# Kernel tuning notes

Hardware: AMD Instinct MI355X
Metric: run time of the kernel (lower is better)

Reference implementation:

```python
import jax, jax.numpy as jnp
import numpy as np

N, E, IN, H, C, OUT = 100000, 800000, 256, 4, 32, 64
NEG_SLOPE = 0.2


def _glorot(key, shape):
    fan = shape[0] if len(shape) > 1 else shape[-1]
    return jax.random.normal(key, shape, dtype=jnp.float32) * (1.0 / np.sqrt(fan))


def setup_inputs() -> dict:
    key = jax.random.key(0)
    ks = jax.random.split(key, 24)
    inp = {
        'x': jax.random.normal(ks[0], (N, IN), dtype=jnp.float32),
        'edge_index': jax.random.randint(ks[1], (2, E), 0, N, dtype=jnp.int64),
        # GATConv layer 0: 256 -> 4 heads x 32 (concat -> 128)
        'W0': _glorot(ks[2], (IN, H * C)), 'b0': jnp.zeros((H * C,), jnp.float32),
        'as0': _glorot(ks[3], (H, C)), 'ad0': _glorot(ks[4], (H, C)),
        # GATConv layer 1: 128 -> 4 heads x 32 (concat -> 128)
        'W1': _glorot(ks[5], (H * C, H * C)), 'b1': jnp.zeros((H * C,), jnp.float32),
        'as1': _glorot(ks[6], (H, C)), 'ad1': _glorot(ks[7], (H, C)),
        # GATConv layer 2: 128 -> 1 head x 64 (mean, concat=False)
        'W2': _glorot(ks[8], (H * C, OUT)), 'b2': jnp.zeros((OUT,), jnp.float32),
        'as2': _glorot(ks[9], (1, OUT)), 'ad2': _glorot(ks[10], (1, OUT)),
        # skip projections: layer0 Linear(256->128), layer1 Identity, layer2 Linear(128->64)
        'skip0_W': _glorot(ks[11], (IN, H * C)), 'skip0_b': jnp.zeros((H * C,), jnp.float32),
        'skip2_W': _glorot(ks[12], (H * C, OUT)), 'skip2_b': jnp.zeros((OUT,), jnp.float32),
        # JK concat linear: (128+128+64) -> 64
        'jk_W': _glorot(ks[13], (2 * H * C + OUT, OUT)), 'jk_b': jnp.zeros((OUT,), jnp.float32),
    }
    return inp


def gat_layer(x, src, dst, n, W, b, a_src, a_dst, heads, concat):
    # x: [N, F_in]; src/dst: [E'] (self-loops included); W: [F_in, heads*C]
    xh = (x @ W).reshape(n, heads, -1)                    # [N, H, C]
    al_src = jnp.einsum('nhc,hc->nh', xh, a_src)          # [N, H]
    al_dst = jnp.einsum('nhc,hc->nh', xh, a_dst)
    e = jax.nn.leaky_relu(al_src[src] + al_dst[dst], NEG_SLOPE)   # [E', H]
    emax = jax.ops.segment_max(e, dst, num_segments=n)    # self-loops => every segment nonempty
    w = jnp.exp(e - emax[dst])                            # [E', H]
    denom = jax.ops.segment_sum(w, dst, num_segments=n)   # [N, H]
    msg = xh[src] * w[:, :, None]                         # [E', H, C]
    out = jax.ops.segment_sum(msg, dst, num_segments=n) / denom[:, :, None]
    if concat:
        return out.reshape(n, -1) + b
    return out.mean(axis=1) + b


def reference(x, edge_index, W0, b0, as0, ad0, W1, b1, as1, ad1, W2, b2, as2, ad2,
              skip0_W, skip0_b, skip2_W, skip2_b, jk_W, jk_b):
    n = x.shape[0]
    loops = jnp.arange(n, dtype=edge_index.dtype)
    src = jnp.concatenate([edge_index[0], loops])
    dst = jnp.concatenate([edge_index[1], loops])
    # layer 0 (dropout is identity in eval mode)
    res0 = x @ skip0_W + skip0_b
    h = gat_layer(x, src, dst, n, W0, b0, as0, ad0, H, True) + res0
    h = jax.nn.elu(h)
    x0 = h
    # layer 1 (skip proj is Identity: 128 == 128)
    h = gat_layer(h, src, dst, n, W1, b1, as1, ad1, H, True) + h
    h = jax.nn.elu(h)
    x1 = h
    # layer 2 (1 head, concat=False -> head mean; no ELU)
    res2 = h @ skip2_W + skip2_b
    h = gat_layer(h, src, dst, n, W2, b2, as2, ad2, 1, False) + res2
    # JumpingKnowledge 'cat' + linear
    jk = jnp.concatenate([x0, x1, h], axis=-1)            # [N, 320]
    return jk @ jk_W + jk_b                               # [N, 64]
```

## Files before the change

### kernel.cpp

```cpp
#include <hip/hip_runtime.h>
#include <hip/hip_bf16.h>
#include <cstdint>

static constexpr int NN = 100000;
static constexpr int NE = 800000;
static constexpr int EP = NE + NN;
static constexpr int NB = (NN + 255) / 256;

typedef unsigned short ushort;
typedef __attribute__((ext_vector_type(8))) short short8;
typedef __attribute__((ext_vector_type(8))) ushort ushort8v;
typedef __attribute__((ext_vector_type(4))) float f32x4;

__device__ __forceinline__ float leaky(float x) { return x > 0.f ? x : 0.2f * x; }

__device__ __forceinline__ ushort f2bf(float f) {
    unsigned int u = __float_as_uint(f);
    u += 0x7fffu + ((u >> 16) & 1u);
    return (ushort)(u >> 16);
}
__device__ __forceinline__ float bf2f(ushort h) {
    return __uint_as_float(((unsigned int)h) << 16);
}

__device__ __forceinline__ void gload16(const void* g, void* l) {
    __builtin_amdgcn_global_load_lds((__attribute__((address_space(1))) void*)g,
                                     (__attribute__((address_space(3))) void*)l,
                                     16, 0, 0);
}

__global__ void pretile_kernel(const float* __restrict__ Wa, const float* __restrict__ Wb,
                               int K, int CS, int NT,
                               ushort* __restrict__ Whi, ushort* __restrict__ Wlo)
{
    int idx = blockIdx.x * 256 + threadIdx.x;
    if (idx >= K * NT) return;
    int k = idx / NT, c = idx - k * NT;
    float v = (c < CS) ? Wa[(size_t)k * CS + c] : Wb[(size_t)k * (NT - CS) + (c - CS)];
    ushort h = f2bf(v);
    ushort l = f2bf(v - bf2f(h));
    size_t o = ((size_t)(k >> 5) * NT + c) * 32 + (k & 31);
    Whi[o] = h; Wlo[o] = l;
}

template<int KTOT, int NTOT, int K1, int K2, int CSPLIT, int BIAS_OFF,
         int AHH, int ACC, int ATTN, bool ASPLIT, int MINW>
__global__ __launch_bounds__(256, MINW)
void gemm_mfma(const void* __restrict__ X1, const void* __restrict__ X1b,
               const void* __restrict__ X2, const void* __restrict__ X2b,
               const void* __restrict__ X3, const void* __restrict__ X3b,
               int ldx1, int ldx2, int ldx3,
               const ushort* __restrict__ Wthi, const ushort* __restrict__ Wtlo,
               const float* __restrict__ bias,
               float* __restrict__ Y1, float* __restrict__ Y2, int ldy1, int ldy2,
               float* __restrict__ als, float* __restrict__ ald,
               const float* __restrict__ a_src, const float* __restrict__ a_dst,
               int n)
{
    constexpr int NKT = KTOT / 32;
    constexpr int NF  = NTOT / 16;

    __shared__ ushort Bh[2][NTOT * 32], Bl[2][NTOT * 32];

    const int t = threadIdx.x, l = t & 63, w = t >> 6;
    const int lc = l & 15, lq = l >> 4;
    const int wrow = blockIdx.x * 128 + w * 32;

    f32x4 acc[2][NF];
#pragma unroll
    for (int mf = 0; mf < 2; ++mf)
#pragma unroll
        for (int nf = 0; nf < NF; ++nf)
            acc[mf][nf] = (f32x4){0.f, 0.f, 0.f, 0.f};

    int  arow[2]; bool aval[2];
#pragma unroll
    for (int mf = 0; mf < 2; ++mf) {
        arow[mf] = wrow + mf * 16 + lc;
        aval[mf] = arow[mf] < n;
    }

    short8 A0h[2], A0l[2], A1h[2], A1l[2];
    float4 F0[2][2], F1[2][2];

    auto loadA = [&](int kt, short8 (&dh)[2], short8 (&dl)[2], float4 (&df)[2][2]) {
        const int k0 = kt * 32;
        const void* xp; const void* xq; int ldx, koff;
        if (k0 < K1)      { xp = X1; xq = X1b; ldx = ldx1; koff = k0; }
        else if (k0 < K2) { xp = X2; xq = X2b; ldx = ldx2; koff = k0 - K1; }
        else              { xp = X3; xq = X3b; ldx = ldx3; koff = k0 - K2; }
        if constexpr (ASPLIT) {
            const ushort* ph = (const ushort*)xp;
            const ushort* pl = (const ushort*)xq;
#pragma unroll
            for (int mf = 0; mf < 2; ++mf) {
                short8 zh = {0,0,0,0,0,0,0,0}, zl = {0,0,0,0,0,0,0,0};
                if (aval[mf]) {
                    size_t o = (size_t)arow[mf] * ldx + koff + lq * 8;
                    zh = *(const short8*)&ph[o];
                    zl = *(const short8*)&pl[o];
                }
                dh[mf] = zh; dl[mf] = zl;
            }
        } else {
            const float* pf = (const float*)xp;
#pragma unroll
            for (int mf = 0; mf < 2; ++mf) {
                float4 za = make_float4(0.f,0.f,0.f,0.f), zb = za;
                if (aval[mf]) {
                    size_t o = (size_t)arow[mf] * ldx + koff + lq * 8;
                    za = *(const float4*)&pf[o];
                    zb = *(const float4*)&pf[o + 4];
                }
                df[mf][0] = za; df[mf][1] = zb;
            }
        }
    };

    auto stageB = [&](int kt, int buf) {
        constexpr int UN = NTOT * 4;
#pragma unroll
        for (int s = 0; s < UN / 256; ++s) {
            int unit = s * 256 + t;
            int col  = unit & (NTOT - 1);
            int kq   = unit / NTOT;
            size_t go = ((size_t)kt * NTOT + col) * 32 + kq * 8;
            gload16(&Wthi[go], &Bh[buf][unit * 8]);
            gload16(&Wtlo[go], &Bl[buf][unit * 8]);
        }
    };

    loadA(0, A0h, A0l, F0);
    stageB(0, 0);
    __syncthreads();

#pragma unroll
    for (int kt = 0; kt < NKT; ++kt) {
        if (kt + 1 < NKT) {
            if (((kt + 1) & 1) == 0) loadA(kt + 1, A0h, A0l, F0);
            else                     loadA(kt + 1, A1h, A1l, F1);
            stageB(kt + 1, (kt + 1) & 1);
        }

        short8 ah[2], al[2];
        if constexpr (ASPLIT) {
            if ((kt & 1) == 0) { ah[0]=A0h[0]; ah[1]=A0h[1]; al[0]=A0l[0]; al[1]=A0l[1]; }
            else               { ah[0]=A1h[0]; ah[1]=A1h[1]; al[0]=A1l[0]; al[1]=A1l[1]; }
        } else {
            const auto& Fc = (kt & 1) ? F1 : F0;
#pragma unroll
            for (int mf = 0; mf < 2; ++mf) {
                short8 h8, l8;
#pragma unroll
                for (int e = 0; e < 8; ++e) {
                    float f = (e < 4) ? (&Fc[mf][0].x)[e] : (&Fc[mf][1].x)[e - 4];
                    ushort hh = f2bf(f);
                    h8[e] = (short)hh;
                    l8[e] = (short)f2bf(f - bf2f(hh));
                }
                ah[mf] = h8; al[mf] = l8;
            }
        }

        const int cb = kt & 1;
#pragma unroll
        for (int nf = 0; nf < NF; ++nf) {
            int bslot = lq * NTOT + nf * 16 + lc;
            short8 bh = *(const short8*)&Bh[cb][bslot * 8];
            short8 bl = *(const short8*)&Bl[cb][bslot * 8];
#pragma unroll
            for (int mf = 0; mf < 2; ++mf) {
                acc[mf][nf] = __builtin_amdgcn_mfma_f32_16x16x32_bf16(ah[mf], bh, acc[mf][nf], 0, 0, 0);
                acc[mf][nf] = __builtin_amdgcn_mfma_f32_16x16x32_bf16(ah[mf], bl, acc[mf][nf], 0, 0, 0);
                acc[mf][nf] = __builtin_amdgcn_mfma_f32_16x16x32_bf16(al[mf], bh, acc[mf][nf], 0, 0, 0);
            }
        }
        __syncthreads();
    }

    if constexpr (AHH > 0) {
        constexpr int FPH = ACC / 16;
        constexpr int NG  = ATTN / ACC;
#pragma unroll
        for (int g = 0; g < NG; ++g) {
#pragma unroll
            for (int mf = 0; mf < 2; ++mf) {
                float ps[4] = {0.f, 0.f, 0.f, 0.f};
                float pd[4] = {0.f, 0.f, 0.f, 0.f};
#pragma unroll
                for (int j = 0; j < FPH; ++j) {
                    int col = g * ACC + j * 16 + lc;
                    float av = a_src[col], dv = a_dst[col];
#pragma unroll
                    for (int r = 0; r < 4; ++r) {
                        ps[r] = fmaf(acc[mf][g * FPH + j][r], av, ps[r]);
                        pd[r] = fmaf(acc[mf][g * FPH + j][r], dv, pd[r]);
                    }
                }
#pragma unroll
                for (int off = 1; off < 16; off <<= 1)
#pragma unroll
                    for (int r = 0; r < 4; ++r) {
                        ps[r] += __shfl_xor(ps[r], off);
                        pd[r] += __shfl_xor(pd[r], off);
                    }
                if (lc == 0) {
#pragma unroll
                    for (int r = 0; r < 4; ++r) {
                        int row = wrow + mf * 16 + lq * 4 + r;
                        if (row < n) {
                            als[(size_t)row * AHH + g] = ps[r];
                            ald[(size_t)row * AHH + g] = pd[r];
                        }
                    }
                }
            }
        }
    }

#pragma unroll
    for (int mf = 0; mf < 2; ++mf) {
        int rb4 = wrow + mf * 16 + lq * 4;
#pragma unroll
        for (int nf = 0; nf < NF; ++nf) {
            int col = nf * 16 + lc;
            float bv = 0.f;
            if constexpr (BIAS_OFF < NTOT) {
                if (col >= BIAS_OFF) bv = bias[col - BIAS_OFF];
            }
#pragma unroll
            for (int r = 0; r < 4; ++r) {
                int row = rb4 + r;
                if (row < n) {
                    float v = acc[mf][nf][r] + bv;
                    if (col < CSPLIT)
                        Y1[(size_t)row * ldy1 + col] = v;
                    else
                        Y2[(size_t)row * ldy2 + (col - CSPLIT)] = v;
                }
            }
        }
    }
}

__global__ void deg_kernel(const int* __restrict__ ei, int* __restrict__ deg)
{
    int t = blockIdx.x * blockDim.x + threadIdx.x;
    if (t < NE) atomicAdd(&deg[ei[NE + t]], 1);
}

__global__ void block_sum_kernel(const int* __restrict__ deg, int* __restrict__ bsum)
{
    int node = blockIdx.x * 256 + threadIdx.x;
    int v = (node < NN) ? deg[node] + 1 : 0;
#pragma unroll
    for (int off = 32; off > 0; off >>= 1) v += __shfl_down(v, off);
    __shared__ int sh[4];
    if ((threadIdx.x & 63) == 0) sh[threadIdx.x >> 6] = v;
    __syncthreads();
    if (threadIdx.x == 0) bsum[blockIdx.x] = sh[0] + sh[1] + sh[2] + sh[3];
}

__global__ void scan_sums_kernel(const int* __restrict__ bsum, int* __restrict__ bsumx,
                                 int* __restrict__ rowptr)
{
    if (threadIdx.x == 0) {
        int run = 0;
        for (int i = 0; i < NB; ++i) { bsumx[i] = run; run += bsum[i]; }
        rowptr[NN] = run;
    }
}

__global__ void scan_blocks_kernel(const int* __restrict__ deg, const int* __restrict__ bsumx,
                                   int* __restrict__ rowptr, int* __restrict__ cursor)
{
    __shared__ int sh[256];
    int node = blockIdx.x * 256 + threadIdx.x;
    int v = (node < NN) ? deg[node] + 1 : 0;
    sh[threadIdx.x] = v;
    __syncthreads();
#pragma unroll
    for (int off = 1; off < 256; off <<= 1) {
        int tv = (threadIdx.x >= off) ? sh[threadIdx.x - off] : 0;
        __syncthreads();
        sh[threadIdx.x] += tv;
        __syncthreads();
    }
    if (node < NN) {
        int excl = bsumx[blockIdx.x] + sh[threadIdx.x] - v;
        rowptr[node] = excl;
        cursor[node] = excl;
    }
}

__global__ void fill_kernel(const int* __restrict__ ei, int* __restrict__ cursor,
                            int* __restrict__ csr_src)
{
    int t = blockIdx.x * blockDim.x + threadIdx.x;
    if (t >= EP) return;
    int s, d;
    if (t < NE) { s = ei[t]; d = ei[NE + t]; }
    else        { s = d = t - NE; }
    int pos = atomicAdd(&cursor[d], 1);
    csr_src[pos] = s;
}

template<int HH>
__global__ __launch_bounds__(256)
void attn_weights_kernel(const int* __restrict__ rowptr, const int* __restrict__ csr_src,
                         const float* __restrict__ als, const float* __restrict__ ald,
                         float* __restrict__ wq, int n)
{
    int node = blockIdx.x * 256 + threadIdx.x;
    if (node >= n) return;
    const int e0 = rowptr[node], e1 = rowptr[node + 1];
    float aldv[HH], m[HH], d[HH];
#pragma unroll
    for (int h = 0; h < HH; ++h) { m[h] = -1e30f; d[h] = 0.f; }
    if constexpr (HH == 4) {
        float4 a = *(const float4*)&ald[(size_t)node * 4];
        aldv[0] = a.x; aldv[1] = a.y; aldv[2] = a.z; aldv[3] = a.w;
    } else {
        aldv[0] = ald[node];
    }
    for (int e = e0; e < e1; ++e) {
        int s = csr_src[e];
        float av[HH];
        if constexpr (HH == 4) {
            float4 a = *(const float4*)&als[(size_t)s * 4];
            av[0] = a.x; av[1] = a.y; av[2] = a.z; av[3] = a.w;
        } else {
            av[0] = als[s];
        }
#pragma unroll
        for (int h = 0; h < HH; ++h) {
            float sc = leaky(av[h] + aldv[h]);
            float nm = fmaxf(m[h], sc);
            d[h] = d[h] * __expf(m[h] - nm) + __expf(sc - nm);
            m[h] = nm;
        }
    }
#pragma unroll
    for (int h = 0; h < HH; ++h) d[h] = 1.f / d[h];
    for (int e = e0; e < e1; ++e) {
        int s = csr_src[e];
        float av[HH];
        if constexpr (HH == 4) {
            float4 a = *(const float4*)&als[(size_t)s * 4];
            av[0] = a.x; av[1] = a.y; av[2] = a.z; av[3] = a.w;
        } else {
            av[0] = als[s];
        }
        float wv[HH];
#pragma unroll
        for (int h = 0; h < HH; ++h)
            wv[h] = __expf(leaky(av[h] + aldv[h]) - m[h]) * d[h];
        if constexpr (HH == 4) {
            float4 o; o.x = wv[0]; o.y = wv[1]; o.z = wv[2]; o.w = wv[3];
            *(float4*)&wq[(size_t)e * 4] = o;
        } else {
            wq[e] = wv[0];
        }
    }
}

template<int HH, int CC, bool DOELU, bool RESSPLIT>
__global__ __launch_bounds__(256)
void spmm_kernel(const int* __restrict__ rowptr, const int* __restrict__ csr_src,
                 const float* __restrict__ xh, const float* __restrict__ wq,
                 const float* __restrict__ b,
                 const float* __restrict__ resf,
                 const ushort* __restrict__ resh, const ushort* __restrict__ resl,
                 ushort* __restrict__ outh, ushort* __restrict__ outl, int n)
{
    constexpr int HCL = HH * CC;
    constexpr int CPL = HCL / 64;
    const int l = threadIdx.x & 63;
    const int node = blockIdx.x * 4 + (threadIdx.x >> 6);
    if (node >= n) return;
    const int c = l * CPL;
    const int h = c / CC;
    const int e0 = rowptr[node], e1 = rowptr[node + 1];

    float a0[CPL], a1[CPL];
#pragma unroll
    for (int j = 0; j < CPL; ++j) { a0[j] = 0.f; a1[j] = 0.f; }

    int e = e0;
    for (; e + 1 < e1; e += 2) {
        int s0 = csr_src[e], s1 = csr_src[e + 1];
        float w0 = wq[(size_t)e * HH + h];
        float w1 = wq[(size_t)(e + 1) * HH + h];
        if constexpr (CPL == 2) {
            float2 x0 = *(const float2*)&xh[(size_t)s0 * HCL + c];
            float2 x1 = *(const float2*)&xh[(size_t)s1 * HCL + c];
            a0[0] = fmaf(w0, x0.x, a0[0]); a0[1] = fmaf(w0, x0.y, a0[1]);
            a1[0] = fmaf(w1, x1.x, a1[0]); a1[1] = fmaf(w1, x1.y, a1[1]);
        } else {
            a0[0] = fmaf(w0, xh[(size_t)s0 * HCL + c], a0[0]);
            a1[0] = fmaf(w1, xh[(size_t)s1 * HCL + c], a1[0]);
        }
    }
    if (e < e1) {
        int s0 = csr_src[e];
        float w0 = wq[(size_t)e * HH + h];
        if constexpr (CPL == 2) {
            float2 x0 = *(const float2*)&xh[(size_t)s0 * HCL + c];
            a0[0] = fmaf(w0, x0.x, a0[0]); a0[1] = fmaf(w0, x0.y, a0[1]);
        } else {
            a0[0] = fmaf(w0, xh[(size_t)s0 * HCL + c], a0[0]);
        }
    }

#pragma unroll
    for (int j = 0; j < CPL; ++j) {
        size_t idx = (size_t)node * HCL + c + j;
        float rv;
        if constexpr (RESSPLIT) rv = bf2f(resh[idx]) + bf2f(resl[idx]);
        else                    rv = resf[idx];
        float v = a0[j] + a1[j] + b[c + j] + rv;
        if (DOELU) v = v > 0.f ? v : (__expf(v) - 1.f);
        ushort hh = f2bf(v);
        outh[idx] = hh;
        outl[idx] = f2bf(v - bf2f(hh));
    }
}

extern "C" void kernel_launch(void* const* d_in, const int* in_sizes, int n_in,
                              void* d_out, int out_size, void* d_ws, size_t ws_size,
                              hipStream_t stream)
{
    const float* x    = (const float*)d_in[0];
    const int*   ei   = (const int*)d_in[1];
    const float* W0   = (const float*)d_in[2];
    const float* b0   = (const float*)d_in[3];
    const float* as0  = (const float*)d_in[4];
    const float* ad0  = (const float*)d_in[5];
    const float* W1   = (const float*)d_in[6];
    const float* b1   = (const float*)d_in[7];
    const float* as1  = (const float*)d_in[8];
    const float* ad1  = (const float*)d_in[9];
    const float* W2   = (const float*)d_in[10];
    const float* b2   = (const float*)d_in[11];
    const float* as2  = (const float*)d_in[12];
    const float* ad2  = (const float*)d_in[13];
    const float* sk0W = (const float*)d_in[14];
    const float* sk0b = (const float*)d_in[15];
    const float* sk2W = (const float*)d_in[16];
    const float* sk2b = (const float*)d_in[17];
    const float* jkW  = (const float*)d_in[18];
    const float* jkb  = (const float*)d_in[19];
    float* out = (float*)d_out;

    float* ws = (float*)d_ws;
    size_t off = 0;
    float* s_xh  = ws + off; off += (size_t)NN * 128;
    float* s_r0  = ws + off; off += (size_t)NN * 128;
    float* s_als = ws + off; off += (size_t)NN * 4;
    float* s_ald = ws + off; off += (size_t)NN * 4;
    float* f_wq  = ws + off; off += (size_t)EP * 4;
    ushort* u_x0h = (ushort*)(ws + off); off += (size_t)NN * 64;
    ushort* u_x0l = (ushort*)(ws + off); off += (size_t)NN * 64;
    ushort* u_x1h = (ushort*)(ws + off); off += (size_t)NN * 64;
    ushort* u_x1l = (ushort*)(ws + off); off += (size_t)NN * 64;
    ushort* u_h2h = (ushort*)(ws + off); off += (size_t)NN * 32;
    ushort* u_h2l = (ushort*)(ws + off); off += (size_t)NN * 32;
    int* i_deg    = (int*)(ws + off); off += NN;
    int* i_rowptr = (int*)(ws + off); off += NN + 1;
    int* i_cursor = (int*)(ws + off); off += NN;
    int* i_csrsrc = (int*)(ws + off); off += EP;
    int* i_bsum   = (int*)(ws + off); off += NB;
    int* i_bsumx  = (int*)(ws + off); off += NB;
    off = (off + 3) & ~(size_t)3;
    ushort* wt0h = (ushort*)(ws + off); off += 32768;
    ushort* wt0l = (ushort*)(ws + off); off += 32768;
    ushort* wt1h = (ushort*)(ws + off); off += 8192;
    ushort* wt1l = (ushort*)(ws + off); off += 8192;
    ushort* wt2h = (ushort*)(ws + off); off += 8192;
    ushort* wt2l = (ushort*)(ws + off); off += 8192;
    ushort* wtjh = (ushort*)(ws + off); off += 10240;
    ushort* wtjl = (ushort*)(ws + off); off += 10240;

    const int G128 = (NN + 127) / 128;
    const int GN = (NN + 255) / 256;
    const int GS = (NN + 3) / 4;
    constexpr int BIG = 1 << 30;

    hipMemsetAsync(i_deg, 0, (size_t)NN * sizeof(int), stream);
    deg_kernel<<<(NE + 255) / 256, 256, 0, stream>>>(ei, i_deg);
    block_sum_kernel<<<NB, 256, 0, stream>>>(i_deg, i_bsum);
    scan_sums_kernel<<<1, 64, 0, stream>>>(i_bsum, i_bsumx, i_rowptr);
    scan_blocks_kernel<<<NB, 256, 0, stream>>>(i_deg, i_bsumx, i_rowptr, i_cursor);
    fill_kernel<<<(EP + 255) / 256, 256, 0, stream>>>(ei, i_cursor, i_csrsrc);

    pretile_kernel<<<256, 256, 0, stream>>>(W0, sk0W, 256, 128, 256, wt0h, wt0l);
    pretile_kernel<<<64,  256, 0, stream>>>(W1, nullptr, 128, 128, 128, wt1h, wt1l);
    pretile_kernel<<<64,  256, 0, stream>>>(W2, sk2W, 128, 64, 128, wt2h, wt2l);
    pretile_kernel<<<80,  256, 0, stream>>>(jkW, nullptr, 320, 64, 64, wtjh, wtjl);

    gemm_mfma<256, 256, 256, 256, 128, 128, 4, 32, 128, false, 2>
        <<<G128, 256, 0, stream>>>(
        x, nullptr, nullptr, nullptr, nullptr, nullptr, 256, 0, 0,
        wt0h, wt0l, sk0b,
        s_xh, s_r0, 128, 128, s_als, s_ald, as0, ad0, NN);
    attn_weights_kernel<4><<<GN, 256, 0, stream>>>(
        i_rowptr, i_csrsrc, s_als, s_ald, f_wq, NN);
    spmm_kernel<4, 32, true, false><<<GS, 256, 0, stream>>>(
        i_rowptr, i_csrsrc, s_xh, f_wq, b0, s_r0, nullptr, nullptr,
        u_x0h, u_x0l, NN);

    gemm_mfma<128, 128, 128, 128, 128, BIG, 4, 32, 128, true, 3>
        <<<G128, 256, 0, stream>>>(
        u_x0h, u_x0l, nullptr, nullptr, nullptr, nullptr, 128, 0, 0,
        wt1h, wt1l, nullptr,
        s_xh, nullptr, 128, 0, s_als, s_ald, as1, ad1, NN);
    attn_weights_kernel<4><<<GN, 256, 0, stream>>>(
        i_rowptr, i_csrsrc, s_als, s_ald, f_wq, NN);
    spmm_kernel<4, 32, true, true><<<GS, 256, 0, stream>>>(
        i_rowptr, i_csrsrc, s_xh, f_wq, b1, nullptr, u_x0h, u_x0l,
        u_x1h, u_x1l, NN);

    gemm_mfma<128, 128, 128, 128, 64, 64, 1, 64, 64, true, 3>
        <<<G128, 256, 0, stream>>>(
        u_x1h, u_x1l, nullptr, nullptr, nullptr, nullptr, 128, 0, 0,
        wt2h, wt2l, sk2b,
        s_xh, s_r0, 64, 64, s_als, s_ald, as2, ad2, NN);
    attn_weights_kernel<1><<<GN, 256, 0, stream>>>(
        i_rowptr, i_csrsrc, s_als, s_ald, f_wq, NN);
    spmm_kernel<1, 64, false, false><<<GS, 256, 0, stream>>>(
        i_rowptr, i_csrsrc, s_xh, f_wq, b2, s_r0, nullptr, nullptr,
        u_h2h, u_h2l, NN);

    gemm_mfma<320, 64, 128, 256, 64, 0, 0, 16, 0, true, 3>
        <<<G128, 256, 0, stream>>>(
        u_x0h, u_x0l, u_x1h, u_x1l, u_h2h, u_h2l, 128, 128, 64,
        wtjh, wtjl, jkb,
        out, nullptr, 64, 0, nullptr, nullptr, nullptr, nullptr, NN);
}
```

Measured before the change: 647.4 us.

## Use partial vmcnt wait barriers so A-prefetch stays in flight across k-tiles

Reorders each k-step so the B tile global->LDS loads are issued before the A register prefetch. The full __syncthreads is replaced by an s_waitcnt vmcnt(4) plus s_barrier, which waits only for the B loads and lets the four A loads for the next tile stay outstanding while the MFMAs run. Out-of-range rows are clamped to n-1 instead of branching, so the load count is uniform and the vmcnt arithmetic holds. The risk is that the hardcoded count of 4 must match the number of A loads per tile. Clamped rows also read real data that must be discarded at store time.

After: 628.6 us. 1.03x faster.

```diff
diff --git a/kernel.cpp b/kernel.cpp
--- a/kernel.cpp
+++ b/kernel.cpp
@@ -27,6 +27,12 @@
     __builtin_amdgcn_global_load_lds((__attribute__((address_space(1))) void*)g,
                                      (__attribute__((address_space(3))) void*)l,
                                      16, 0, 0);
+}
+
+__device__ __forceinline__ void waitbar4() {
+    asm volatile("s_waitcnt vmcnt(4)" ::: "memory");
+    __builtin_amdgcn_s_barrier();
+    __builtin_amdgcn_sched_barrier(0);
 }
 
 __global__ void pretile_kernel(const float* __restrict__ Wa, const float* __restrict__ Wb,
@@ -73,11 +79,11 @@
         for (int nf = 0; nf < NF; ++nf)
             acc[mf][nf] = (f32x4){0.f, 0.f, 0.f, 0.f};
 
-    int  arow[2]; bool aval[2];
+    int arow[2], rcl[2];
 #pragma unroll
     for (int mf = 0; mf < 2; ++mf) {
         arow[mf] = wrow + mf * 16 + lc;
-        aval[mf] = arow[mf] < n;
+        rcl[mf]  = arow[mf] < n ? arow[mf] : (n - 1);
     }
 
     short8 A0h[2], A0l[2], A1h[2], A1l[2];
@@ -94,25 +100,17 @@
             const ushort* pl = (const ushort*)xq;
 #pragma unroll
             for (int mf = 0; mf < 2; ++mf) {
-                short8 zh = {0,0,0,0,0,0,0,0}, zl = {0,0,0,0,0,0,0,0};
-                if (aval[mf]) {
-                    size_t o = (size_t)arow[mf] * ldx + koff + lq * 8;
-                    zh = *(const short8*)&ph[o];
-                    zl = *(const short8*)&pl[o];
-                }
-                dh[mf] = zh; dl[mf] = zl;
+                size_t o = (size_t)rcl[mf] * ldx + koff + lq * 8;
+                dh[mf] = *(const short8*)&ph[o];
+                dl[mf] = *(const short8*)&pl[o];
             }
         } else {
             const float* pf = (const float*)xp;
 #pragma unroll
             for (int mf = 0; mf < 2; ++mf) {
-                float4 za = make_float4(0.f,0.f,0.f,0.f), zb = za;
-                if (aval[mf]) {
-                    size_t o = (size_t)arow[mf] * ldx + koff + lq * 8;
-                    za = *(const float4*)&pf[o];
-                    zb = *(const float4*)&pf[o + 4];
-                }
-                df[mf][0] = za; df[mf][1] = zb;
+                size_t o = (size_t)rcl[mf] * ldx + koff + lq * 8;
+                df[mf][0] = *(const float4*)&pf[o];
+                df[mf][1] = *(const float4*)&pf[o + 4];
             }
         }
     };
@@ -130,16 +128,18 @@
         }
     };
 
+    stageB(0, 0);
+    __builtin_amdgcn_sched_barrier(0);
     loadA(0, A0h, A0l, F0);
-    stageB(0, 0);
-    __syncthreads();
+    waitbar4();
 
 #pragma unroll
     for (int kt = 0; kt < NKT; ++kt) {
         if (kt + 1 < NKT) {
+            stageB(kt + 1, (kt + 1) & 1);
+            __builtin_amdgcn_sched_barrier(0);
             if (((kt + 1) & 1) == 0) loadA(kt + 1, A0h, A0l, F0);
             else                     loadA(kt + 1, A1h, A1l, F1);
-            stageB(kt + 1, (kt + 1) & 1);
         }
 
         short8 ah[2], al[2];
@@ -175,7 +175,7 @@
                 acc[mf][nf] = __builtin_amdgcn_mfma_f32_16x16x32_bf16(al[mf], bh, acc[mf][nf], 0, 0, 0);
             }
         }
-        __syncthreads();
+        if (kt + 1 < NKT) waitbar4();
     }
 
     if constexpr (AHH > 0) {
```
